# Kernel optimization log

Hardware: AMD Instinct MI355X
Metric: run time of the kernel (lower is better)

## Reference

```python
import jax, jax.numpy as jnp
import numpy as np

MAX_PTS = 512     # _MAX_POINTS_PER_BOX
MIN_PTS = 4       # _MIN_POINTS_FOR_NET


def setup_inputs() -> dict:
    key = jax.random.key(0)
    ks = jax.random.split(key, 8)
    N, A = 131072, 1024
    # LiDAR-like cloud over a 100m x 100m plot, heights up to 30m
    points = jax.random.uniform(ks[0], (N, 3)) * jnp.array([100.0, 100.0, 30.0])
    # anchors: (x, y, z_c, w, l, h); z_c is unused by the box test in the source
    cxy = jax.random.uniform(ks[1], (A, 2)) * 100.0
    wl = 2.0 + jax.random.uniform(ks[2], (A, 2)) * 4.0      # 2..6 m footprint
    h = 20.0 + jax.random.uniform(ks[3], (A, 1)) * 15.0     # 20..35 m tall
    anchors = jnp.concatenate([cxy, jnp.zeros((A, 1)), wl, h], axis=-1)
    W1 = jax.random.normal(ks[4], (3, 64)) * 0.3
    W2 = jax.random.normal(ks[5], (64, 128)) * 0.1
    Wc = jax.random.normal(ks[6], (128, 1)) * 0.1
    Wr = jax.random.normal(ks[7], (128, 4)) * 0.1
    return {
        'points': points, 'anchors': anchors,
        'W1': W1, 'b1': jnp.zeros(64), 'W2': W2, 'b2': jnp.zeros(128),
        'Wc': Wc, 'bc': jnp.zeros(1), 'Wr': Wr, 'br': jnp.zeros(4),
    }


def reference(points, anchors, W1, b1, W2, b2, Wc, bc, Wr, br):
    # points: (N,3)  anchors: (A,6) = (x, y, z_c, w, l, h)
    N = points.shape[0]
    x, y = anchors[:, 0], anchors[:, 1]
    w, l, h = anchors[:, 3], anchors[:, 4], anchors[:, 5]
    px, py, pz = points[:, 0], points[:, 1], points[:, 2]
    # point-in-box test, (A, N)  -- mirrors _subsample_points_in_box
    inside = ((px[None] >= (x - w / 2)[:, None]) & (px[None] <= (x + w / 2)[:, None]) &
              (py[None] >= (y - l / 2)[:, None]) & (py[None] <= (y + l / 2)[:, None]) &
              (pz[None] >= 0.0) & (pz[None] <= h[:, None]))
    count = inside.sum(-1)                                   # (A,)
    # first MAX_PTS inside-points per anchor (deterministic subsample)
    score = jnp.where(inside, -jnp.arange(N, dtype=jnp.float32)[None], -jnp.inf)
    _, idx = jax.lax.top_k(score, MAX_PTS)                   # (A, K)
    # repeat-padding as in _pad_windows_to_batch: cycle through the n points
    pos = jnp.arange(MAX_PTS)[None] % jnp.maximum(count, 1)[:, None]
    gidx = jnp.take_along_axis(idx, pos, axis=1)             # (A, K)
    pts = points[gidx]                                       # (A, K, 3)
    # normalize xy relative to anchor center (z untouched)
    pts = pts - jnp.stack([x, y, jnp.zeros_like(x)], -1)[:, None, :]
    # stage1 PointNet head: per-point MLP -> max-pool -> cls/reg linears
    f = jax.nn.relu(pts @ W1 + b1)
    f = jax.nn.relu(f @ W2 + b2)                             # (A, K, 128)
    g = f.max(axis=1)                                        # (A, 128)
    cls = g @ Wc + bc                                        # (A, 1)
    reg = g @ Wr + br                                        # (A, 4)
    # anchors with < MIN_PTS points get zeroed outputs (as in the source)
    valid = (count >= MIN_PTS)[:, None].astype(pts.dtype)
    return jnp.concatenate([cls, reg], axis=-1) * valid      # (A, 5)
```

## Files before the change

kernel.cpp:

```cpp
#include <hip/hip_runtime.h>
#include <hip/hip_bf16.h>
#include <stdint.h>

#define NPTS   131072
#define NANCH  1024
#define GRID   25
#define NCELL  (GRID*GRID)
#define CINV   0.25f
#define MAXP   512
#define MINP   4
#define IDXCAP 1024
#define HB     128
#define PPB    (NPTS/HB)

typedef __attribute__((ext_vector_type(8))) short bf16x8;
typedef __attribute__((ext_vector_type(4))) float f32x4;

__device__ __forceinline__ int cell_of(float px, float py) {
    int cx = (int)(px * CINV); cx = cx < 0 ? 0 : (cx > GRID-1 ? GRID-1 : cx);
    int cy = (int)(py * CINV); cy = cy < 0 ? 0 : (cy > GRID-1 ? GRID-1 : cy);
    return cy * GRID + cx;
}

__device__ __forceinline__ unsigned short f2bf(float f) {
    union { float f; uint32_t u; } v; v.f = f;
    return (unsigned short)((v.u + 0x7fff + ((v.u >> 16) & 1)) >> 16);
}


__global__ __launch_bounds__(256) void k_hist(const float* __restrict__ pts,
                                              int* __restrict__ blockhist,
                                              int* __restrict__ cellrank) {
    __shared__ int lh[NCELL];
    const int b = blockIdx.x, tid = threadIdx.x;
    for (int i = tid; i < NCELL; i += 256) lh[i] = 0;
    __syncthreads();
    const int base = b * PPB;
    #pragma unroll
    for (int k = 0; k < PPB/256; k++) {
        int i = base + k*256 + tid;
        int c = cell_of(pts[3*i], pts[3*i+1]);
        int r = atomicAdd(&lh[c], 1);
        cellrank[i] = c | (r << 10);
    }
    __syncthreads();
    for (int i = tid; i < NCELL; i += 256) blockhist[b*NCELL + i] = lh[i];
}

__global__ __launch_bounds__(1024) void k_scan(const int* __restrict__ blockhist,
                                               int* __restrict__ blockpre,
                                               int* __restrict__ cstart,
                                               const float* __restrict__ W2,
                                               unsigned short* __restrict__ w2tg) {
    __shared__ int sc[1024];
    const int c = threadIdx.x;
    int acc = 0;
    if (c < NCELL) {
        #pragma unroll 8
        for (int b = 0; b < HB; b++) {
            int v = blockhist[b*NCELL + c];
            blockpre[b*NCELL + c] = acc;
            acc += v;
        }
    } else if (c >= 640 && c < 896) {
        int u = c - 640;
        int col = u >> 1, ks = (u & 1) * 32;
        #pragma unroll
        for (int kk = 0; kk < 32; kk += 2) {
            int k = ks + kk;
            uint32_t pk = (uint32_t)f2bf(W2[k*128 + col])
                        | ((uint32_t)f2bf(W2[(k+1)*128 + col]) << 16);
            *(uint32_t*)&w2tg[col*64 + k] = pk;
        }
    }
    sc[c] = (c < NCELL) ? acc : 0;
    __syncthreads();
    for (int off = 1; off < 1024; off <<= 1) {
        int x = (c >= off) ? sc[c - off] : 0;
        __syncthreads();
        sc[c] += x;
        __syncthreads();
    }
    if (c < NCELL) cstart[c] = sc[c] - acc;
    if (c == NCELL-1) cstart[NCELL] = sc[c];
}

__global__ __launch_bounds__(256) void k_scatter(const float* __restrict__ pts,
                                                 const int* __restrict__ cellrank,
                                                 const int* __restrict__ blockpre,
                                                 const int* __restrict__ cstart,
                                                 float4* __restrict__ binned) {
    __shared__ int lbase[NCELL];
    const int b = blockIdx.x, tid = threadIdx.x;
    for (int i = tid; i < NCELL; i += 256)
        lbase[i] = cstart[i] + blockpre[b*NCELL + i];
    __syncthreads();
    const int base = b * PPB;
    #pragma unroll
    for (int k = 0; k < PPB/256; k++) {
        int i = base + k*256 + tid;
        int v = cellrank[i];
        int c = v & 1023, r = v >> 10;
        binned[lbase[c] + r] = make_float4(pts[3*i], pts[3*i+1], pts[3*i+2],
                                           __int_as_float(i));
    }
}


__launch_bounds__(256, 4)
__global__ void k_main(const float* __restrict__ pts,
                       const float* __restrict__ anch,
                       const float* __restrict__ W1, const float* __restrict__ b1,
                       const float* __restrict__ b2,
                       const float* __restrict__ Wc, const float* __restrict__ bc,
                       const float* __restrict__ Wr, const float* __restrict__ br,
                       const unsigned short* __restrict__ w2tg,
                       const float4* __restrict__ binned,
                       const int* __restrict__ cstart,
                       float* __restrict__ out) {
    __shared__ float spx[MAXP], spy[MAXP], spz[MAXP];
    __shared__ int   sidx[IDXCAP];
    __shared__ unsigned short h1b[64*64];
    __shared__ float w1s[3][64];
    __shared__ float b1s[64];
    __shared__ float gmax2[128];
    __shared__ int   s_cnt;

    const int a    = blockIdx.x;
    const int tid  = threadIdx.x;
    const int lane = tid & 63;
    const int wv   = tid >> 6;
    const int l15  = lane & 15;
    const int kb   = (lane >> 4) * 8;

    const float ax = anch[6*a],   ay = anch[6*a+1];
    const float w  = anch[6*a+3], l  = anch[6*a+4], hh = anch[6*a+5];
    const float hw = w * 0.5f, hl = l * 0.5f;
    const float x0 = ax - hw, x1 = ax + hw, y0 = ay - hl, y1 = ay + hl;

    bf16x8 b00, b01, b10, b11;
    {
        const int c0 = wv*16 + l15, c1 = c0 + 64;
        b00 = *(const bf16x8*)&w2tg[c0*64 + kb];
        b01 = *(const bf16x8*)&w2tg[c0*64 + 32 + kb];
        b10 = *(const bf16x8*)&w2tg[c1*64 + kb];
        b11 = *(const bf16x8*)&w2tg[c1*64 + 32 + kb];
    }

    if (tid == 0) s_cnt = 0;
    if (tid < 64) {
        w1s[0][tid] = W1[tid]; w1s[1][tid] = W1[64+tid]; w1s[2][tid] = W1[128+tid];
        b1s[tid] = b1[tid];
    }
    __syncthreads();

    int cx0 = (int)floorf(x0 * CINV); if (cx0 < 0) cx0 = 0;
    int cx1 = (int)floorf(x1 * CINV); if (cx1 > GRID-1) cx1 = GRID-1;
    int cy0 = (int)floorf(y0 * CINV); if (cy0 < 0) cy0 = 0;
    int cy1 = (int)floorf(y1 * CINV); if (cy1 > GRID-1) cy1 = GRID-1;

    for (int cy = cy0; cy <= cy1; cy++)
        for (int cx = cx0; cx <= cx1; cx++) {
            int c = cy * GRID + cx;
            int p0 = cstart[c], p1 = cstart[c+1];
            for (int base = p0; base < p1; base += 256) {
                int i = base + tid;
                bool ins = false;
                float4 P;
                if (i < p1) {
                    P = binned[i];
                    ins = (P.x >= x0) & (P.x <= x1) & (P.y >= y0) & (P.y <= y1)
                        & (P.z >= 0.f) & (P.z <= hh);
                }
                unsigned long long m = __ballot(ins);
                int wbase;
                if (lane == 0) wbase = atomicAdd(&s_cnt, __popcll(m));
                wbase = __shfl(wbase, 0);
                if (ins) {
                    int pos = wbase + __popcll(m & ((1ull << lane) - 1ull));
                    if (pos < MAXP)   { spx[pos] = P.x - ax; spy[pos] = P.y - ay; spz[pos] = P.z; }
                    if (pos < IDXCAP) sidx[pos] = __float_as_int(P.w);
                }
            }
        }
    __syncthreads();
    const int cnt = s_cnt;

    if (cnt < MINP) {
        if (tid < 5) out[5*a + tid] = 0.f;
        return;
    }

    if (cnt > MAXP) {
        for (int i = cnt + tid; i < IDXCAP; i += 256) sidx[i] = 0x7fffffff;
        __syncthreads();
        for (int k = 2; k <= IDXCAP; k <<= 1) {
            for (int j = k >> 1; j > 0; j >>= 1) {
                #pragma unroll
                for (int e = 0; e < IDXCAP/256; e++) {
                    int i = tid + e*256;
                    int partner = i ^ j;
                    if (partner > i) {
                        int va = sidx[i], vb = sidx[partner];
                        bool up = ((i & k) == 0);
                        if ((va > vb) == up) { sidx[i] = vb; sidx[partner] = va; }
                    }
                }
                __syncthreads();
            }
        }
        for (int i = tid; i < MAXP; i += 256) {
            int idx = sidx[i];
            spx[i] = pts[3*idx]   - ax;
            spy[i] = pts[3*idx+1] - ay;
            spz[i] = pts[3*idx+2];
        }
        __syncthreads();
    }

    const int gathered = cnt < MAXP ? cnt : MAXP;
    const int padded   = (gathered + 63) & ~63;
    for (int i = gathered + tid; i < padded; i += 256) {
        spx[i] = spx[0]; spy[i] = spy[0]; spz[i] = spz[0];
    }
    __syncthreads();

    float gm0 = -INFINITY, gm1 = -INFINITY;
    const int pairid = tid & 31;
    const int rowg   = tid >> 5;

    for (int pb = 0; pb < padded; pb += 64) {
        #pragma unroll
        for (int pass = 0; pass < 8; pass++) {
            int row = pass*8 + rowg;
            int p = pb + row;
            float qx = spx[p], qy = spy[p], qz = spz[p];
            int d0 = pairid * 2;
            float v0 = fmaf(qz, w1s[2][d0],   fmaf(qy, w1s[1][d0],   fmaf(qx, w1s[0][d0],   b1s[d0])));
            float v1 = fmaf(qz, w1s[2][d0+1], fmaf(qy, w1s[1][d0+1], fmaf(qx, w1s[0][d0+1], b1s[d0+1])));
            v0 = fmaxf(v0, 0.f); v1 = fmaxf(v1, 0.f);
            uint32_t pk = (uint32_t)f2bf(v0) | ((uint32_t)f2bf(v1) << 16);
            int idx = (row*64 + d0) ^ ((row & 7) << 3);
            *(uint32_t*)&h1b[idx] = pk;
        }
        __syncthreads();

        #pragma unroll
        for (int mt = 0; mt < 4; mt++) {
            int r = mt*16 + l15;
            int ai0 = (r*64 +      kb) ^ ((r & 7) << 3);
            int ai1 = (r*64 + 32 + kb) ^ ((r & 7) << 3);
            bf16x8 a0 = *(const bf16x8*)&h1b[ai0];
            bf16x8 a1 = *(const bf16x8*)&h1b[ai1];
            f32x4 z = {0.f, 0.f, 0.f, 0.f};
            f32x4 c;
            c = __builtin_amdgcn_mfma_f32_16x16x32_bf16(a0, b00, z, 0, 0, 0);
            c = __builtin_amdgcn_mfma_f32_16x16x32_bf16(a1, b01, c, 0, 0, 0);
            gm0 = fmaxf(gm0, fmaxf(fmaxf(c[0], c[1]), fmaxf(c[2], c[3])));
            c = __builtin_amdgcn_mfma_f32_16x16x32_bf16(a0, b10, z, 0, 0, 0);
            c = __builtin_amdgcn_mfma_f32_16x16x32_bf16(a1, b11, c, 0, 0, 0);
            gm1 = fmaxf(gm1, fmaxf(fmaxf(c[0], c[1]), fmaxf(c[2], c[3])));
        }
        __syncthreads();
    }

    gm0 = fmaxf(gm0, __shfl_xor(gm0, 16)); gm0 = fmaxf(gm0, __shfl_xor(gm0, 32));
    gm1 = fmaxf(gm1, __shfl_xor(gm1, 16)); gm1 = fmaxf(gm1, __shfl_xor(gm1, 32));
    if (lane < 16) {
        gmax2[wv*16     + lane] = gm0;
        gmax2[(wv+4)*16 + lane] = gm1;
    }
    __syncthreads();
    if (tid < 128) gmax2[tid] = fmaxf(gmax2[tid] + b2[tid], 0.f);
    __syncthreads();

    if (tid < 5) {
        const float* Wv; float bias; int stride;
        if (tid == 0) { Wv = Wc;            bias = bc[0];      stride = 1; }
        else          { Wv = Wr + (tid-1);  bias = br[tid-1];  stride = 4; }
        float acc = bias;
        for (int i = 0; i < 128; i++) acc = fmaf(gmax2[i], Wv[i*stride], acc);
        out[5*a + tid] = acc;
    }
}


extern "C" void kernel_launch(void* const* d_in, const int* in_sizes, int n_in,
                              void* d_out, int out_size, void* d_ws, size_t ws_size,
                              hipStream_t stream) {
    const float* pts  = (const float*)d_in[0];
    const float* anch = (const float*)d_in[1];
    const float* W1   = (const float*)d_in[2];
    const float* b1   = (const float*)d_in[3];
    const float* W2   = (const float*)d_in[4];
    const float* b2   = (const float*)d_in[5];
    const float* Wc   = (const float*)d_in[6];
    const float* bc   = (const float*)d_in[7];
    const float* Wr   = (const float*)d_in[8];
    const float* br   = (const float*)d_in[9];
    float* out = (float*)d_out;

    char* ws = (char*)d_ws;
    float4*         binned    = (float4*)ws;
    int*            blockhist = (int*)(ws + (size_t)NPTS*16);
    int*            blockpre  = blockhist + HB*NCELL;
    int*            cstart    = blockpre  + HB*NCELL;
    int*            cellrank  = cstart + 1024;
    unsigned short* w2tg      = (unsigned short*)(cellrank + NPTS);

    k_hist   <<<HB, 256, 0, stream>>>(pts, blockhist, cellrank);
    k_scan   <<<1, 1024, 0, stream>>>(blockhist, blockpre, cstart, W2, w2tg);
    k_scatter<<<HB, 256, 0, stream>>>(pts, cellrank, blockpre, cstart, binned);
    k_main   <<<NANCH, 256, 0, stream>>>(pts, anch, W1, b1, b2, Wc, bc, Wr, br,
                                         w2tg, binned, cstart, out);
}
```

Before: 109.4 us.

## Fuse hist/scan/scatter into one kernel with last-block grid sync; vectorize layer-1

```diff
diff --git a/kernel.cpp b/kernel.cpp
--- a/kernel.cpp
+++ b/kernel.cpp
@@ -28,81 +28,99 @@
 }
 
 
-__global__ __launch_bounds__(256) void k_hist(const float* __restrict__ pts,
-                                              int* __restrict__ blockhist,
-                                              int* __restrict__ cellrank) {
+__global__ __launch_bounds__(256) void k_bin(const float* __restrict__ pts,
+                                             const float* __restrict__ W2,
+                                             int* __restrict__ blockhist,
+                                             int* __restrict__ blockpre,
+                                             int* __restrict__ cstart,
+                                             unsigned short* __restrict__ w2tg,
+                                             float4* __restrict__ binned,
+                                             int* __restrict__ sync_ctr,
+                                             int* __restrict__ rel_flag) {
     __shared__ int lh[NCELL];
+    __shared__ int tsum[256];
+    __shared__ int s_last;
     const int b = blockIdx.x, tid = threadIdx.x;
+
     for (int i = tid; i < NCELL; i += 256) lh[i] = 0;
     __syncthreads();
+
+    float px[4], py[4], pz[4]; int pc[4], pr[4];
     const int base = b * PPB;
     #pragma unroll
-    for (int k = 0; k < PPB/256; k++) {
+    for (int k = 0; k < 4; k++) {
         int i = base + k*256 + tid;
-        int c = cell_of(pts[3*i], pts[3*i+1]);
-        int r = atomicAdd(&lh[c], 1);
-        cellrank[i] = c | (r << 10);
+        px[k] = pts[3*i]; py[k] = pts[3*i+1]; pz[k] = pts[3*i+2];
+        pc[k] = cell_of(px[k], py[k]);
+        pr[k] = atomicAdd(&lh[pc[k]], 1);
     }
     __syncthreads();
     for (int i = tid; i < NCELL; i += 256) blockhist[b*NCELL + i] = lh[i];
-}
-
-__global__ __launch_bounds__(1024) void k_scan(const int* __restrict__ blockhist,
-                                               int* __restrict__ blockpre,
-                                               int* __restrict__ cstart,
-                                               const float* __restrict__ W2,
-                                               unsigned short* __restrict__ w2tg) {
-    __shared__ int sc[1024];
-    const int c = threadIdx.x;
-    int acc = 0;
-    if (c < NCELL) {
-        #pragma unroll 8
-        for (int b = 0; b < HB; b++) {
-            int v = blockhist[b*NCELL + c];
-            blockpre[b*NCELL + c] = acc;
-            acc += v;
-        }
-    } else if (c >= 640 && c < 896) {
-        int u = c - 640;
-        int col = u >> 1, ks = (u & 1) * 32;
+
+    if (b == 0) {
+        int col = tid >> 1, ks = (tid & 1) * 32;
         #pragma unroll
         for (int kk = 0; kk < 32; kk += 2) {
-            int k = ks + kk;
-            uint32_t pk = (uint32_t)f2bf(W2[k*128 + col])
-                        | ((uint32_t)f2bf(W2[(k+1)*128 + col]) << 16);
-            *(uint32_t*)&w2tg[col*64 + k] = pk;
-        }
-    }
-    sc[c] = (c < NCELL) ? acc : 0;
-    __syncthreads();
-    for (int off = 1; off < 1024; off <<= 1) {
-        int x = (c >= off) ? sc[c - off] : 0;
-        __syncthreads();
-        sc[c] += x;
-        __syncthreads();
-    }
-    if (c < NCELL) cstart[c] = sc[c] - acc;
-    if (c == NCELL-1) cstart[NCELL] = sc[c];
-}
-
-__global__ __launch_bounds__(256) void k_scatter(const float* __restrict__ pts,
-                                                 const int* __restrict__ cellrank,
-                                                 const int* __restrict__ blockpre,
-                                                 const int* __restrict__ cstart,
-                                                 float4* __restrict__ binned) {
-    __shared__ int lbase[NCELL];
-    const int b = blockIdx.x, tid = threadIdx.x;
-    for (int i = tid; i < NCELL; i += 256)
-        lbase[i] = cstart[i] + blockpre[b*NCELL + i];
-    __syncthreads();
-    const int base = b * PPB;
+            int k2 = ks + kk;
+            uint32_t pk = (uint32_t)f2bf(W2[k2*128 + col])
+                        | ((uint32_t)f2bf(W2[(k2+1)*128 + col]) << 16);
+            *(uint32_t*)&w2tg[col*64 + k2] = pk;
+        }
+    }
+
+    __threadfence();
+    if (tid == 0) s_last = (atomicAdd(sync_ctr, 1) == HB - 1);
+    __syncthreads();
+
+    if (s_last) {
+        #pragma unroll
+        for (int u = 0; u < 3; u++) {
+            int c = tid + u*256;
+            if (c < NCELL) {
+                int a2 = 0;
+                #pragma unroll 8
+                for (int bb = 0; bb < HB; bb++) {
+                    int v = blockhist[bb*NCELL + c];
+                    blockpre[bb*NCELL + c] = a2;
+                    a2 += v;
+                }
+                lh[c] = a2;
+            }
+        }
+        __syncthreads();
+        int c0 = 3*tid;
+        int v0 = (c0   < NCELL) ? lh[c0]   : 0;
+        int v1 = (c0+1 < NCELL) ? lh[c0+1] : 0;
+        int v2 = (c0+2 < NCELL) ? lh[c0+2] : 0;
+        tsum[tid] = v0 + v1 + v2;
+        __syncthreads();
+        for (int off = 1; off < 256; off <<= 1) {
+            int x = (tid >= off) ? tsum[tid - off] : 0;
+            __syncthreads();
+            tsum[tid] += x;
+            __syncthreads();
+        }
+        int excl = tid ? tsum[tid-1] : 0;
+        if (c0   < NCELL) cstart[c0]   = excl;
+        if (c0+1 < NCELL) cstart[c0+1] = excl + v0;
+        if (c0+2 < NCELL) cstart[c0+2] = excl + v0 + v1;
+        if (tid == 255) cstart[NCELL] = tsum[255];
+        __threadfence();
+        if (tid == 0) atomicExch(rel_flag, 1);
+    } else {
+        if (tid == 0) {
+            while (atomicAdd(rel_flag, 0) == 0) { __builtin_amdgcn_s_sleep(2); }
+        }
+        __syncthreads();
+        __threadfence();
+    }
+
     #pragma unroll
-    for (int k = 0; k < PPB/256; k++) {
-        int i = base + k*256 + tid;
-        int v = cellrank[i];
-        int c = v & 1023, r = v >> 10;
-        binned[lbase[c] + r] = make_float4(pts[3*i], pts[3*i+1], pts[3*i+2],
-                                           __int_as_float(i));
+    for (int k = 0; k < 4; k++) {
+        int c = pc[k];
+        int pos = cstart[c] + blockpre[b*NCELL + c] + pr[k];
+        binned[pos] = make_float4(px[k], py[k], pz[k],
+                                  __int_as_float(base + k*256 + tid));
     }
 }
 
@@ -225,23 +243,35 @@
     }
     __syncthreads();
 
+    const int dg    = tid & 15;
+    const int rowst = (tid >> 4) & 15;
+    float wxr[4], wyr[4], wzr[4], bbr[4];
+    #pragma unroll
+    for (int j = 0; j < 4; j++) {
+        int d = 4*dg + j;
+        wxr[j] = w1s[0][d]; wyr[j] = w1s[1][d]; wzr[j] = w1s[2][d]; bbr[j] = b1s[d];
+    }
+
     float gm0 = -INFINITY, gm1 = -INFINITY;
-    const int pairid = tid & 31;
-    const int rowg   = tid >> 5;
 
     for (int pb = 0; pb < padded; pb += 64) {
         #pragma unroll
-        for (int pass = 0; pass < 8; pass++) {
-            int row = pass*8 + rowg;
-            int p = pb + row;
-            float qx = spx[p], qy = spy[p], qz = spz[p];
-            int d0 = pairid * 2;
-            float v0 = fmaf(qz, w1s[2][d0],   fmaf(qy, w1s[1][d0],   fmaf(qx, w1s[0][d0],   b1s[d0])));
-            float v1 = fmaf(qz, w1s[2][d0+1], fmaf(qy, w1s[1][d0+1], fmaf(qx, w1s[0][d0+1], b1s[d0+1])));
+        for (int p = 0; p < 4; p++) {
+            int row = p*16 + rowst;
+            float qx = spx[pb+row], qy = spy[pb+row], qz = spz[pb+row];
+            float v0 = fmaf(qz, wzr[0], fmaf(qy, wyr[0], fmaf(qx, wxr[0], bbr[0])));
+            float v1 = fmaf(qz, wzr[1], fmaf(qy, wyr[1], fmaf(qx, wxr[1], bbr[1])));
+            float v2 = fmaf(qz, wzr[2], fmaf(qy, wyr[2], fmaf(qx, wxr[2], bbr[2])));
+            float v3 = fmaf(qz, wzr[3], fmaf(qy, wyr[3], fmaf(qx, wxr[3], bbr[3])));
             v0 = fmaxf(v0, 0.f); v1 = fmaxf(v1, 0.f);
-            uint32_t pk = (uint32_t)f2bf(v0) | ((uint32_t)f2bf(v1) << 16);
-            int idx = (row*64 + d0) ^ ((row & 7) << 3);
-            *(uint32_t*)&h1b[idx] = pk;
+            v2 = fmaxf(v2, 0.f); v3 = fmaxf(v3, 0.f);
+            __hip_bfloat162 lo = __float22bfloat162_rn(float2{v0, v1});
+            __hip_bfloat162 hi = __float22bfloat162_rn(float2{v2, v3});
+            uint2 val;
+            val.x = *(uint32_t*)&lo;
+            val.y = *(uint32_t*)&hi;
+            int idx = (row*64 + 4*dg) ^ ((row & 7) << 3);
+            *(uint2*)&h1b[idx] = val;
         }
         __syncthreads();
 
@@ -305,12 +335,12 @@
     int*            blockhist = (int*)(ws + (size_t)NPTS*16);
     int*            blockpre  = blockhist + HB*NCELL;
     int*            cstart    = blockpre  + HB*NCELL;
-    int*            cellrank  = cstart + 1024;
-    unsigned short* w2tg      = (unsigned short*)(cellrank + NPTS);
-
-    k_hist   <<<HB, 256, 0, stream>>>(pts, blockhist, cellrank);
-    k_scan   <<<1, 1024, 0, stream>>>(blockhist, blockpre, cstart, W2, w2tg);
-    k_scatter<<<HB, 256, 0, stream>>>(pts, cellrank, blockpre, cstart, binned);
-    k_main   <<<NANCH, 256, 0, stream>>>(pts, anch, W1, b1, b2, Wc, bc, Wr, br,
-                                         w2tg, binned, cstart, out);
-}
+    unsigned short* w2tg      = (unsigned short*)(ws + 2739712);
+    int*            syncp     = (int*)(ws + 2756096);
+
+    hipMemsetAsync(syncp, 0, 16, stream);
+    k_bin  <<<HB, 256, 0, stream>>>(pts, W2, blockhist, blockpre, cstart,
+                                    w2tg, binned, syncp, syncp + 1);
+    k_main <<<NANCH, 256, 0, stream>>>(pts, anch, W1, b1, b2, Wc, bc, Wr, br,
+                                       w2tg, binned, cstart, out);
+}
```

New measurement: 136.6 us. 24.8% more time.
